# Kernel tuning notes

Hardware: AMD Instinct MI355X
Metric: run time of the kernel (lower is better)

The kernel has to match this reference:

```python
import jax, jax.numpy as jnp
import numpy as np

N_HEADS = 16  # matches init_kwargs

def setup_inputs() -> dict:
    key = jax.random.key(0)
    ks = jax.random.split(key, 7)
    B, S, D = 2, 2048, 2048
    return {
        "query": jax.random.normal(ks[0], (B, S, D), jnp.float32),
        "key":   jax.random.normal(ks[1], (B, S, D), jnp.float32),
        "value": jax.random.normal(ks[2], (B, S, D), jnp.float32),
        "Wq": jax.random.normal(ks[3], (D, D), jnp.float32) * 0.02,
        "Wk": jax.random.normal(ks[4], (D, D), jnp.float32) * 0.02,
        "Wv": jax.random.normal(ks[5], (D, D), jnp.float32) * 0.02,
        "Wo": jax.random.normal(ks[6], (D, D), jnp.float32) * 0.02,
        "block_size": 64,
    }

def reference(query, key, value, Wq, Wk, Wv, Wo, block_size):
    # Faithful to the torch module: softmax is applied INDEPENDENTLY per
    # k-block (no online-softmax rescaling) and block outputs are summed.
    B, S, D = query.shape
    H = N_HEADS
    hd = D // H
    nb = S // block_size  # number of k-blocks (S is a multiple of block_size)
    scale = jnp.asarray(np.sqrt(hd), query.dtype)

    # nn.Linear(bias=False): y = x @ W.T
    q = (query @ Wq.T).reshape(B, S, H, hd).transpose(0, 2, 1, 3)  # [B,H,S,hd]
    k = (key   @ Wk.T).reshape(B, S, H, hd).transpose(0, 2, 1, 3)
    v = (value @ Wv.T).reshape(B, S, H, hd).transpose(0, 2, 1, 3)

    kb = k.reshape(B, H, nb, block_size, hd)  # k-blocks
    vb = v.reshape(B, H, nb, block_size, hd)

    scores = jnp.einsum('bhsd,bhnkd->bhsnk', q, kb) / scale  # [B,H,S,nb,bs]
    attn = jax.nn.softmax(scores, axis=-1)  # per-block softmax (as in source)
    out = jnp.einsum('bhsnk,bhnkd->bhsd', attn, vb)  # sum over blocks

    attn_weights = attn.reshape(B, H, S, S)  # full materialized attn matrix
    out = out.transpose(0, 2, 1, 3).reshape(B, S, D) @ Wo.T
    return out, attn_weights
```

## Files before the change

kernel.cpp:

```cpp
#include <hip/hip_runtime.h>

typedef unsigned short u16;
typedef unsigned int u32;
typedef __attribute__((ext_vector_type(8))) __bf16 bf16x8;
typedef __attribute__((ext_vector_type(4))) float f32x4;

__device__ __forceinline__ void gl_lds16(const void* g, void* l) {
  __builtin_amdgcn_global_load_lds((__attribute__((address_space(1))) void*)g,
                                   (__attribute__((address_space(3))) void*)l,
                                   16, 0, 0);
}

__device__ __forceinline__ u16 f2bf(float f) {
  u32 x = __builtin_bit_cast(u32, f);
  return (u16)((x + 0x7fffu + ((x >> 16) & 1u)) >> 16);
}

__global__ __launch_bounds__(256) void cvt_all(
    const float* __restrict__ q, const float* __restrict__ k, const float* __restrict__ v,
    const float* __restrict__ wq, const float* __restrict__ wk, const float* __restrict__ wv,
    const float* __restrict__ wo,
    u16* __restrict__ xq, u16* __restrict__ xk, u16* __restrict__ xv,
    u16* __restrict__ owq, u16* __restrict__ owk, u16* __restrict__ owv,
    u16* __restrict__ owo) {
  int bid = blockIdx.x;
  const float* src;
  u16* dst;
  int chunk;
  if (bid < 12288) {
    int t = bid >> 12;
    chunk = bid & 4095;
    src = (t == 0) ? q : (t == 1) ? k : v;
    dst = (t == 0) ? xq : (t == 1) ? xk : xv;
  } else {
    int b2 = bid - 12288;
    int t = b2 >> 11;
    chunk = b2 & 2047;
    src = (t == 0) ? wq : (t == 1) ? wk : (t == 2) ? wv : wo;
    dst = (t == 0) ? owq : (t == 1) ? owk : (t == 2) ? owv : owo;
  }
  int i = (chunk * 256 + (int)threadIdx.x) * 8;
  const float4* p = (const float4*)(src + i);
  float4 a = p[0], b = p[1];
  uint4 u;
  u.x = f2bf(a.x) | ((u32)f2bf(a.y) << 16);
  u.y = f2bf(a.z) | ((u32)f2bf(a.w) << 16);
  u.z = f2bf(b.x) | ((u32)f2bf(b.y) << 16);
  u.w = f2bf(b.z) | ((u32)f2bf(b.w) << 16);
  *(uint4*)(dst + i) = u;
}

template <bool F32OUT>
__device__ __forceinline__ void gemm_body(const u16* __restrict__ A, const u16* __restrict__ B,
                                          void* __restrict__ Cptr, int m0, int n0, int N, int K,
                                          u16* As, u16* Bs) {
  const int tid = threadIdx.x;
  const int lane = tid & 63, w = tid >> 6;
  const int wm = (w & 1) * 64, wn = (w >> 1) * 64;
  const int fm = lane & 15, quad = lane >> 4;
  const int sr = lane >> 2, sc = lane & 3;
  f32x4 acc[4][4] = {};
  for (int k0 = 0; k0 < K; k0 += 32) {
    __syncthreads();
    for (int i = w; i < 8; i += 4) {
      int r = i * 16 + sr;
      int ca = sc ^ ((r >> 1) & 3);
      gl_lds16(A + (size_t)(m0 + r) * K + k0 + ca * 8, &As[i * 512]);
      gl_lds16(B + (size_t)(n0 + r) * K + k0 + ca * 8, &Bs[i * 512]);
    }
    __syncthreads();
    bf16x8 af[4], bfr[4];
#pragma unroll
    for (int t = 0; t < 4; t++) {
      int ra = wm + t * 16 + fm;
      af[t] = *(const bf16x8*)&As[ra * 32 + ((quad ^ ((ra >> 1) & 3)) << 3)];
      int rb = wn + t * 16 + fm;
      bfr[t] = *(const bf16x8*)&Bs[rb * 32 + ((quad ^ ((rb >> 1) & 3)) << 3)];
    }
#pragma unroll
    for (int mt = 0; mt < 4; mt++)
#pragma unroll
      for (int nt = 0; nt < 4; nt++)
        acc[mt][nt] = __builtin_amdgcn_mfma_f32_16x16x32_bf16(af[mt], bfr[nt], acc[mt][nt], 0, 0, 0);
  }
  const int er = quad * 4;
#pragma unroll
  for (int mt = 0; mt < 4; mt++)
#pragma unroll
    for (int nt = 0; nt < 4; nt++)
#pragma unroll
      for (int r = 0; r < 4; r++) {
        size_t idx = (size_t)(m0 + wm + mt * 16 + er + r) * N + (n0 + wn + nt * 16 + fm);
        if (F32OUT) ((float*)Cptr)[idx] = acc[mt][nt][r];
        else        ((u16*)Cptr)[idx] = f2bf(acc[mt][nt][r]);
      }
}

__global__ __launch_bounds__(256, 2)
void gemm_qkv(const u16* __restrict__ Xq, const u16* __restrict__ Wqb, u16* __restrict__ Qb,
              const u16* __restrict__ Xk, const u16* __restrict__ Wkb, u16* __restrict__ Kb,
              const u16* __restrict__ Xv, const u16* __restrict__ Wvb, u16* __restrict__ Vt) {
  __shared__ u16 As[128 * 32];
  __shared__ u16 Bs[128 * 32];
  const int flat = blockIdx.x + (blockIdx.y << 9);
  const int work = (flat & 7) * 192 + (flat >> 3);
  const int z = work >> 9, bid = work & 511;
  const u16 *A, *B;
  u16* C;
  int N, m0, n0;
  if (z == 0) {
    A = Xq; B = Wqb; C = Qb; N = 2048;
    m0 = (bid >> 4) << 7; n0 = (bid & 15) << 7;
  } else if (z == 1) {
    A = Xk; B = Wkb; C = Kb; N = 2048;
    m0 = (bid >> 4) << 7; n0 = (bid & 15) << 7;
  } else {
    A = Wvb; B = Xv; C = Vt; N = 4096;
    m0 = (bid >> 5) << 7; n0 = (bid & 31) << 7;
  }
  gemm_body<false>(A, B, C, m0, n0, N, 2048, As, Bs);
}

__global__ __launch_bounds__(256, 2)
void gemm_out(const u16* __restrict__ A, const u16* __restrict__ B, float* __restrict__ C) {
  __shared__ u16 As[128 * 32];
  __shared__ u16 Bs[128 * 32];
  const int flat = blockIdx.x + (blockIdx.y << 4);
  const int work = ((flat & 7) << 6) + (flat >> 3);
  const int m0 = (work >> 4) << 7, n0 = (work & 15) << 7;
  gemm_body<true>(A, B, C, m0, n0, 2048, 2048, As, Bs);
}

__global__ __launch_bounds__(512, 4)
void attn_kernel(const u16* __restrict__ Q, const u16* __restrict__ Kmat,
                 const u16* __restrict__ Vt, float* __restrict__ attn_out,
                 u16* __restrict__ ctx) {
  __shared__ u16 Ks[2][64 * 128];
  __shared__ u16 Vts[2][128 * 64];
  __shared__ u16 Ps[128 * 64];
  const int tid = threadIdx.x, lane = tid & 63, w = tid >> 6;
  const int flat = blockIdx.x + (blockIdx.y << 4) + (blockIdx.z << 8);
  const int work = ((flat & 7) << 6) + (flat >> 3);
  const int qt = work & 15, h = (work >> 4) & 15, b = work >> 8;
  const int q0 = qt * 128;
  const int fm = lane & 15, quad = lane >> 4;
  const float c_e2 = 0.088388347648318447f * 1.4426950408889634f;

  bf16x8 qf[4];
  {
    const u16* Qg = Q + (size_t)(b * 2048 + q0 + w * 16 + fm) * 2048 + h * 128;
#pragma unroll
    for (int kt = 0; kt < 4; kt++)
      qf[kt] = *(const bf16x8*)(Qg + kt * 32 + quad * 8);
  }
  f32x4 cacc[8] = {};
  const u16* Kg = Kmat + (size_t)b * 2048 * 2048 + h * 128;
  const u16* Vg = Vt + (size_t)(h * 128) * 4096 + b * 2048;
  const int krl = lane >> 4, kcl = lane & 15;
  const int vrl = lane >> 3, vcl = lane & 7;

#define STAGE(buf, kbb)                                                              \
  for (int i = w; i < 16; i += 8) {                                                  \
    int rk = i * 4 + krl;                                                            \
    int ck = kcl ^ (rk & 15);                                                        \
    gl_lds16(Kg + (size_t)((kbb) * 64 + rk) * 2048 + ck * 8, &Ks[(buf)][i * 512]);   \
    int rv = i * 8 + vrl;                                                            \
    int cv = vcl ^ (rv & 7);                                                         \
    gl_lds16(Vg + (size_t)rv * 4096 + (kbb) * 64 + cv * 8, &Vts[(buf)][i * 512]);    \
  }

  STAGE(0, 0)
  asm volatile("s_waitcnt vmcnt(0)" ::: "memory");
  __builtin_amdgcn_s_barrier();

  for (int kb = 0; kb < 32; kb++) {
    const int cur = kb & 1;
    if (kb < 31) { STAGE(cur ^ 1, kb + 1) }

    f32x4 sacc[4] = {};
#pragma unroll
    for (int kt = 0; kt < 4; kt++) {
      bf16x8 kf[4];
#pragma unroll
      for (int nt = 0; nt < 4; nt++) {
        int rk = nt * 16 + fm;
        int ck = (kt * 4 + quad) ^ (rk & 15);
        kf[nt] = *(const bf16x8*)&Ks[cur][rk * 128 + ck * 8];
      }
      __builtin_amdgcn_s_setprio(1);
#pragma unroll
      for (int nt = 0; nt < 4; nt++)
        sacc[nt] = __builtin_amdgcn_mfma_f32_16x16x32_bf16(qf[kt], kf[nt], sacc[nt], 0, 0, 0);
      __builtin_amdgcn_s_setprio(0);
    }

#pragma unroll
    for (int r = 0; r < 4; r++) {
      float v0 = sacc[0][r], v1 = sacc[1][r], v2 = sacc[2][r], v3 = sacc[3][r];
      float mx = fmaxf(fmaxf(v0, v1), fmaxf(v2, v3));
      mx = fmaxf(mx, __shfl_xor(mx, 1));
      mx = fmaxf(mx, __shfl_xor(mx, 2));
      mx = fmaxf(mx, __shfl_xor(mx, 4));
      mx = fmaxf(mx, __shfl_xor(mx, 8));
      float e0 = exp2f((v0 - mx) * c_e2);
      float e1 = exp2f((v1 - mx) * c_e2);
      float e2 = exp2f((v2 - mx) * c_e2);
      float e3 = exp2f((v3 - mx) * c_e2);
      float s = e0 + e1 + e2 + e3;
      s += __shfl_xor(s, 1);
      s += __shfl_xor(s, 2);
      s += __shfl_xor(s, 4);
      s += __shfl_xor(s, 8);
      float inv = __builtin_amdgcn_rcpf(s);
      float p0 = e0 * inv, p1 = e1 * inv, p2 = e2 * inv, p3 = e3 * inv;
      int row = w * 16 + quad * 4 + r;
      size_t ob = ((size_t)((b * 16 + h) * 2048 + q0 + row)) * 2048 + kb * 64;
      attn_out[ob + fm] = p0;
      attn_out[ob + 16 + fm] = p1;
      attn_out[ob + 32 + fm] = p2;
      attn_out[ob + 48 + fm] = p3;
      int rw7 = row & 7, fh = fm >> 3, fl = fm & 7;
      u16* pp = &Ps[row * 64];
      pp[(((0 + fh) ^ rw7) << 3) + fl] = f2bf(p0);
      pp[(((2 + fh) ^ rw7) << 3) + fl] = f2bf(p1);
      pp[(((4 + fh) ^ rw7) << 3) + fl] = f2bf(p2);
      pp[(((6 + fh) ^ rw7) << 3) + fl] = f2bf(p3);
    }

#pragma unroll
    for (int kt = 0; kt < 2; kt++) {
      bf16x8 pa, vb[8];
      {
        int rp = w * 16 + fm;
        int cp = (kt * 4 + quad) ^ (rp & 7);
        pa = *(const bf16x8*)&Ps[rp * 64 + cp * 8];
      }
#pragma unroll
      for (int nt = 0; nt < 8; nt++) {
        int rv = nt * 16 + fm;
        int cv = (kt * 4 + quad) ^ (rv & 7);
        vb[nt] = *(const bf16x8*)&Vts[cur][rv * 64 + cv * 8];
      }
      __builtin_amdgcn_s_setprio(1);
#pragma unroll
      for (int nt = 0; nt < 8; nt++)
        cacc[nt] = __builtin_amdgcn_mfma_f32_16x16x32_bf16(pa, vb[nt], cacc[nt], 0, 0, 0);
      __builtin_amdgcn_s_setprio(0);
    }

    if (kb < 31) {
      asm volatile("s_waitcnt vmcnt(0)" ::: "memory");
      __builtin_amdgcn_s_barrier();
    }
  }
#undef STAGE

#pragma unroll
  for (int nt = 0; nt < 8; nt++)
#pragma unroll
    for (int r = 0; r < 4; r++) {
      int row = q0 + w * 16 + quad * 4 + r;
      int col = h * 128 + nt * 16 + fm;
      ctx[(size_t)(b * 2048 + row) * 2048 + col] = f2bf(cacc[nt][r]);
    }
}

extern "C" void kernel_launch(void* const* d_in, const int* in_sizes, int n_in,
                              void* d_out, int out_size, void* d_ws, size_t ws_size,
                              hipStream_t stream) {
  const float* query = (const float*)d_in[0];
  const float* key   = (const float*)d_in[1];
  const float* value = (const float*)d_in[2];
  const float* Wq = (const float*)d_in[3];
  const float* Wk = (const float*)d_in[4];
  const float* Wv = (const float*)d_in[5];
  const float* Wo = (const float*)d_in[6];

  float* out  = (float*)d_out;
  float* attn = out + (size_t)8388608;

  u16* ws  = (u16*)d_ws;
  u16* wqb = ws;
  u16* wkb = wqb + 4194304;
  u16* wvb = wkb + 4194304;
  u16* wob = wvb + 4194304;
  u16* Qb  = wob + 4194304;
  u16* Kb  = Qb + 8388608;
  u16* Vtb = Kb + 8388608;
  u16* ctx = Vtb + 8388608;
  u16* Xq = (u16*)attn;
  u16* Xk = Xq + 8388608;
  u16* Xv = Xk + 8388608;

  cvt_all<<<20480, 256, 0, stream>>>(query, key, value, Wq, Wk, Wv, Wo,
                                     Xq, Xk, Xv, wqb, wkb, wvb, wob);

  gemm_qkv<<<dim3(512, 3, 1), 256, 0, stream>>>(Xq, wqb, Qb, Xk, wkb, Kb, Xv, wvb, Vtb);

  attn_kernel<<<dim3(16, 16, 2), 512, 0, stream>>>(Qb, Kb, Vtb, attn, ctx);

  gemm_out<<<dim3(16, 32, 1), 256, 0, stream>>>(ctx, wob, out);
}
```

Baseline: 980.8 us.

## Rewrite projection GEMMs with 8-wave 256x128 tiles and double-buffered LDS prefetch

Replaces the 4-wave 128x128 GEMM body with an 8-wave 256x128 tile using K=64 steps. LDS is double-buffered and the next tile's global-to-LDS loads are interleaved with MFMA phases, using s_setprio and a new XOR swizzle. The intent is to hide global load latency and cut per-step sync overhead in the QKV and output projections. The cost is higher LDS use per block (96KB) and fewer blocks, and gemm_out8 launches only 256 blocks, which may underfill the GPU.

```diff
diff --git a/kernel.cpp b/kernel.cpp
--- a/kernel.cpp
+++ b/kernel.cpp
@@ -51,84 +51,155 @@
 }
 
 template <bool F32OUT>
-__device__ __forceinline__ void gemm_body(const u16* __restrict__ A, const u16* __restrict__ B,
-                                          void* __restrict__ Cptr, int m0, int n0, int N, int K,
-                                          u16* As, u16* Bs) {
+__device__ __forceinline__ void gemm8_body(const u16* __restrict__ A, const u16* __restrict__ B,
+                                           void* __restrict__ Cptr, int m0, int n0, int N, int K,
+                                           u16 (*As)[16384], u16 (*Bs)[8192]) {
   const int tid = threadIdx.x;
   const int lane = tid & 63, w = tid >> 6;
-  const int wm = (w & 1) * 64, wn = (w >> 1) * 64;
+  const int wr = w >> 1, wc = w & 1;
   const int fm = lane & 15, quad = lane >> 4;
-  const int sr = lane >> 2, sc = lane & 3;
+  const int sr = lane >> 3, sc = lane & 7;
   f32x4 acc[4][4] = {};
-  for (int k0 = 0; k0 < K; k0 += 32) {
-    __syncthreads();
-    for (int i = w; i < 8; i += 4) {
-      int r = i * 16 + sr;
-      int ca = sc ^ ((r >> 1) & 3);
-      gl_lds16(A + (size_t)(m0 + r) * K + k0 + ca * 8, &As[i * 512]);
-      gl_lds16(B + (size_t)(n0 + r) * K + k0 + ca * 8, &Bs[i * 512]);
-    }
-    __syncthreads();
-    bf16x8 af[4], bfr[4];
-#pragma unroll
-    for (int t = 0; t < 4; t++) {
-      int ra = wm + t * 16 + fm;
-      af[t] = *(const bf16x8*)&As[ra * 32 + ((quad ^ ((ra >> 1) & 3)) << 3)];
-      int rb = wn + t * 16 + fm;
-      bfr[t] = *(const bf16x8*)&Bs[rb * 32 + ((quad ^ ((rb >> 1) & 3)) << 3)];
-    }
-#pragma unroll
-    for (int mt = 0; mt < 4; mt++)
-#pragma unroll
-      for (int nt = 0; nt < 4; nt++)
-        acc[mt][nt] = __builtin_amdgcn_mfma_f32_16x16x32_bf16(af[mt], bfr[nt], acc[mt][nt], 0, 0, 0);
-  }
-  const int er = quad * 4;
-#pragma unroll
-  for (int mt = 0; mt < 4; mt++)
-#pragma unroll
-    for (int nt = 0; nt < 4; nt++)
+
+#define STAGE_A8(buf, kt1, i) \
+  gl_lds16(A + (size_t)(m0 + (i) * 8 + sr) * K + (kt1) * 64 + ((sc ^ sr) << 3), &As[buf][(i) * 512])
+#define STAGE_B8(buf, kt1, i) \
+  gl_lds16(B + (size_t)(n0 + (i) * 8 + sr) * K + (kt1) * 64 + ((sc ^ sr) << 3), &Bs[buf][(i) * 512])
+
+  for (int i = w; i < 32; i += 8) STAGE_A8(0, 0, i);
+  for (int i = w; i < 16; i += 8) STAGE_B8(0, 0, i);
+  asm volatile("s_waitcnt vmcnt(0)" ::: "memory");
+  __builtin_amdgcn_s_barrier();
+
+  const int NKT = K >> 6;
+  for (int kt = 0; kt < NKT; kt++) {
+    const int cur = kt & 1, nxt = cur ^ 1;
+    const bool pf = (kt + 1 < NKT);
+    bf16x8 af[2][2][2], bf[2][2][2];
+
+#pragma unroll
+    for (int f = 0; f < 2; f++)
+#pragma unroll
+      for (int ks = 0; ks < 2; ks++) {
+        int ra = wr * 64 + f * 16 + fm;
+        af[0][f][ks] = *(const bf16x8*)&As[cur][ra * 64 + (((ks * 4 + quad) ^ (ra & 7)) << 3)];
+        int rb = wc * 64 + f * 16 + fm;
+        bf[0][f][ks] = *(const bf16x8*)&Bs[cur][rb * 64 + (((ks * 4 + quad) ^ (rb & 7)) << 3)];
+      }
+    if (pf) {
+      for (int i = w; i < 32; i += 8) STAGE_A8(nxt, kt + 1, i);
+    }
+    __builtin_amdgcn_s_barrier();
+    __builtin_amdgcn_s_setprio(1);
+#pragma unroll
+    for (int mf = 0; mf < 2; mf++)
+#pragma unroll
+      for (int nf = 0; nf < 2; nf++)
+#pragma unroll
+        for (int ks = 0; ks < 2; ks++)
+          acc[mf][nf] = __builtin_amdgcn_mfma_f32_16x16x32_bf16(af[0][mf][ks], bf[0][nf][ks], acc[mf][nf], 0, 0, 0);
+    __builtin_amdgcn_s_setprio(0);
+
+#pragma unroll
+    for (int f = 0; f < 2; f++)
+#pragma unroll
+      for (int ks = 0; ks < 2; ks++) {
+        int ra = wr * 64 + 32 + f * 16 + fm;
+        af[1][f][ks] = *(const bf16x8*)&As[cur][ra * 64 + (((ks * 4 + quad) ^ (ra & 7)) << 3)];
+      }
+    if (pf) {
+      for (int i = w; i < 16; i += 8) STAGE_B8(nxt, kt + 1, i);
+    }
+    __builtin_amdgcn_s_barrier();
+    __builtin_amdgcn_s_setprio(1);
+#pragma unroll
+    for (int mf = 0; mf < 2; mf++)
+#pragma unroll
+      for (int nf = 0; nf < 2; nf++)
+#pragma unroll
+        for (int ks = 0; ks < 2; ks++)
+          acc[2 + mf][nf] = __builtin_amdgcn_mfma_f32_16x16x32_bf16(af[1][mf][ks], bf[0][nf][ks], acc[2 + mf][nf], 0, 0, 0);
+    __builtin_amdgcn_s_setprio(0);
+
+#pragma unroll
+    for (int f = 0; f < 2; f++)
+#pragma unroll
+      for (int ks = 0; ks < 2; ks++) {
+        int rb = wc * 64 + 32 + f * 16 + fm;
+        bf[1][f][ks] = *(const bf16x8*)&Bs[cur][rb * 64 + (((ks * 4 + quad) ^ (rb & 7)) << 3)];
+      }
+    __builtin_amdgcn_s_barrier();
+    __builtin_amdgcn_s_setprio(1);
+#pragma unroll
+    for (int mf = 0; mf < 2; mf++)
+#pragma unroll
+      for (int nf = 0; nf < 2; nf++)
+#pragma unroll
+        for (int ks = 0; ks < 2; ks++)
+          acc[mf][2 + nf] = __builtin_amdgcn_mfma_f32_16x16x32_bf16(af[0][mf][ks], bf[1][nf][ks], acc[mf][2 + nf], 0, 0, 0);
+    __builtin_amdgcn_s_setprio(0);
+
+    __builtin_amdgcn_s_setprio(1);
+#pragma unroll
+    for (int mf = 0; mf < 2; mf++)
+#pragma unroll
+      for (int nf = 0; nf < 2; nf++)
+#pragma unroll
+        for (int ks = 0; ks < 2; ks++)
+          acc[2 + mf][2 + nf] = __builtin_amdgcn_mfma_f32_16x16x32_bf16(af[1][mf][ks], bf[1][nf][ks], acc[2 + mf][2 + nf], 0, 0, 0);
+    __builtin_amdgcn_s_setprio(0);
+
+    if (pf) asm volatile("s_waitcnt vmcnt(0)" ::: "memory");
+    __builtin_amdgcn_s_barrier();
+  }
+#undef STAGE_A8
+#undef STAGE_B8
+
+#pragma unroll
+  for (int fi = 0; fi < 4; fi++)
+#pragma unroll
+    for (int fj = 0; fj < 4; fj++)
 #pragma unroll
       for (int r = 0; r < 4; r++) {
-        size_t idx = (size_t)(m0 + wm + mt * 16 + er + r) * N + (n0 + wn + nt * 16 + fm);
-        if (F32OUT) ((float*)Cptr)[idx] = acc[mt][nt][r];
-        else        ((u16*)Cptr)[idx] = f2bf(acc[mt][nt][r]);
-      }
-}
-
-__global__ __launch_bounds__(256, 2)
-void gemm_qkv(const u16* __restrict__ Xq, const u16* __restrict__ Wqb, u16* __restrict__ Qb,
-              const u16* __restrict__ Xk, const u16* __restrict__ Wkb, u16* __restrict__ Kb,
-              const u16* __restrict__ Xv, const u16* __restrict__ Wvb, u16* __restrict__ Vt) {
-  __shared__ u16 As[128 * 32];
-  __shared__ u16 Bs[128 * 32];
-  const int flat = blockIdx.x + (blockIdx.y << 9);
-  const int work = (flat & 7) * 192 + (flat >> 3);
-  const int z = work >> 9, bid = work & 511;
+        size_t idx = (size_t)(m0 + wr * 64 + fi * 16 + quad * 4 + r) * N + (n0 + wc * 64 + fj * 16 + fm);
+        if (F32OUT) ((float*)Cptr)[idx] = acc[fi][fj][r];
+        else        ((u16*)Cptr)[idx] = f2bf(acc[fi][fj][r]);
+      }
+}
+
+__global__ __launch_bounds__(512, 2)
+void gemm_qkv8(const u16* __restrict__ Xq, const u16* __restrict__ Wqb, u16* __restrict__ Qb,
+               const u16* __restrict__ Xk, const u16* __restrict__ Wkb, u16* __restrict__ Kb,
+               const u16* __restrict__ Xv, const u16* __restrict__ Wvb, u16* __restrict__ Vt) {
+  __shared__ u16 As[2][16384];
+  __shared__ u16 Bs[2][8192];
+  const int flat = blockIdx.x;
+  const int work = (flat & 7) * 96 + (flat >> 3);
+  const int z = work >> 8, r = work & 255;
   const u16 *A, *B;
   u16* C;
   int N, m0, n0;
   if (z == 0) {
     A = Xq; B = Wqb; C = Qb; N = 2048;
-    m0 = (bid >> 4) << 7; n0 = (bid & 15) << 7;
+    m0 = (r >> 4) << 8; n0 = (r & 15) << 7;
   } else if (z == 1) {
     A = Xk; B = Wkb; C = Kb; N = 2048;
-    m0 = (bid >> 4) << 7; n0 = (bid & 15) << 7;
+    m0 = (r >> 4) << 8; n0 = (r & 15) << 7;
   } else {
     A = Wvb; B = Xv; C = Vt; N = 4096;
-    m0 = (bid >> 5) << 7; n0 = (bid & 31) << 7;
-  }
-  gemm_body<false>(A, B, C, m0, n0, N, 2048, As, Bs);
-}
-
-__global__ __launch_bounds__(256, 2)
-void gemm_out(const u16* __restrict__ A, const u16* __restrict__ B, float* __restrict__ C) {
-  __shared__ u16 As[128 * 32];
-  __shared__ u16 Bs[128 * 32];
-  const int flat = blockIdx.x + (blockIdx.y << 4);
-  const int work = ((flat & 7) << 6) + (flat >> 3);
-  const int m0 = (work >> 4) << 7, n0 = (work & 15) << 7;
-  gemm_body<true>(A, B, C, m0, n0, 2048, 2048, As, Bs);
+    m0 = (r >> 5) << 8; n0 = (r & 31) << 7;
+  }
+  gemm8_body<false>(A, B, C, m0, n0, N, 2048, As, Bs);
+}
+
+__global__ __launch_bounds__(512, 2)
+void gemm_out8(const u16* __restrict__ A, const u16* __restrict__ B, float* __restrict__ C) {
+  __shared__ u16 As[2][16384];
+  __shared__ u16 Bs[2][8192];
+  const int flat = blockIdx.x;
+  const int work = ((flat & 7) << 5) + (flat >> 3);
+  const int m0 = (work >> 4) << 8, n0 = (work & 15) << 7;
+  gemm8_body<true>(A, B, C, m0, n0, 2048, 2048, As, Bs);
 }
 
 __global__ __launch_bounds__(512, 4)
@@ -295,9 +366,9 @@
   cvt_all<<<20480, 256, 0, stream>>>(query, key, value, Wq, Wk, Wv, Wo,
                                      Xq, Xk, Xv, wqb, wkb, wvb, wob);
 
-  gemm_qkv<<<dim3(512, 3, 1), 256, 0, stream>>>(Xq, wqb, Qb, Xk, wkb, Kb, Xv, wvb, Vtb);
+  gemm_qkv8<<<768, 512, 0, stream>>>(Xq, wqb, Qb, Xk, wkb, Kb, Xv, wvb, Vtb);
 
   attn_kernel<<<dim3(16, 16, 2), 512, 0, stream>>>(Qb, Kb, Vtb, attn, ctx);
 
-  gemm_out<<<dim3(16, 32, 1), 256, 0, stream>>>(ctx, wob, out);
-}
+  gemm_out8<<<256, 512, 0, stream>>>(ctx, wob, out);
+}
```

New measurement: 1.019 ms. 1.04x slower.
